# Performance work log

Measured on AMD Instinct MI355X. Metric: run time of the kernel, lower is better.

Reference implementation:

```python
import jax, jax.numpy as jnp
import numpy as np

DIM = 2048
N_HEADS = 32
N_KV_HEADS = 8
HEAD_DIM = 64
REPEATS = N_HEADS // N_KV_HEADS
SLIDING_WINDOW = 1024
EPS = 1e-6
B, T = 2, 2048


def _alibi_slopes(n):
    # n_heads=32 is a power of 2
    r = 2.0 ** (-8.0 / n)
    return jnp.asarray([r ** i for i in range(n)], dtype=jnp.float32)


def _rms_norm(x, w, eps):
    # RMSNorm over the last (flattened heads*head_dim) axis
    var = jnp.mean(x * x, axis=-1, keepdims=True)
    return x * jax.lax.rsqrt(var + eps) * w


def setup_inputs() -> dict:
    key = jax.random.key(0)
    ks = jax.random.split(key, 6)
    s = 0.02
    return {
        "x": jax.random.normal(ks[0], (B, T, DIM), jnp.float32),
        "wq": jax.random.normal(ks[1], (N_HEADS * HEAD_DIM, DIM), jnp.float32) * s,
        "wk": jax.random.normal(ks[2], (N_KV_HEADS * HEAD_DIM, DIM), jnp.float32) * s,
        "wv": jax.random.normal(ks[3], (N_KV_HEADS * HEAD_DIM, DIM), jnp.float32) * s,
        "wo": jax.random.normal(ks[4], (DIM, N_HEADS * HEAD_DIM), jnp.float32) * s,
        "q_norm_w": jnp.ones((N_HEADS * HEAD_DIM,), jnp.float32),
        "k_norm_w": jnp.ones((N_KV_HEADS * HEAD_DIM,), jnp.float32),
    }


def reference(x, wq, wk, wv, wo, q_norm_w, k_norm_w):
    bsz, seqlen, _ = x.shape
    xq = _rms_norm(x @ wq.T, q_norm_w, EPS)
    xk = _rms_norm(x @ wk.T, k_norm_w, EPS)
    xv = x @ wv.T
    xq = xq.reshape(bsz, seqlen, N_HEADS, HEAD_DIM).transpose(0, 2, 1, 3)  # b h t d
    xk = xk.reshape(bsz, seqlen, N_KV_HEADS, HEAD_DIM).transpose(0, 2, 1, 3)
    xv = xv.reshape(bsz, seqlen, N_KV_HEADS, HEAD_DIM).transpose(0, 2, 1, 3)
    # GQA: repeat_interleave kv heads
    xk = jnp.repeat(xk, REPEATS, axis=1)
    xv = jnp.repeat(xv, REPEATS, axis=1)

    pos = jnp.arange(seqlen)
    dist = pos[None, :] - pos[:, None]                     # [t,s] = s - t (<=0 on causal side)
    slopes = _alibi_slopes(N_HEADS)
    alibi = slopes[:, None, None] * dist.astype(jnp.float32)  # [h,t,s]
    allowed = (dist <= 0) & (dist >= -SLIDING_WINDOW)      # causal + sliding window
    bias = jnp.where(allowed[None], alibi, -jnp.inf)       # [h,t,s]

    scale = 1.0 / jnp.sqrt(jnp.asarray(HEAD_DIM, jnp.float32))
    scores = jnp.einsum("bhtd,bhsd->bhts", xq, xk) * scale + bias[None]
    attn = jax.nn.softmax(scores, axis=-1)
    out = jnp.einsum("bhts,bhsd->bhtd", attn, xv)          # [b,h,t,d]
    out = out.transpose(0, 2, 1, 3).reshape(bsz, seqlen, N_HEADS * HEAD_DIM)
    return out @ wo.T
```

## Files before the change

kernel.cpp:

```cpp
#include <hip/hip_runtime.h>


typedef _Float16 f16;
typedef __attribute__((ext_vector_type(8))) _Float16 f16x8;
typedef __attribute__((ext_vector_type(4))) _Float16 f16x4;
typedef __attribute__((ext_vector_type(4))) float f32x4;

#define T_ 2048
#define NH 32
#define NKV 8
#define HD 64
#define WINDOW 1024
#define EPS_ 1e-6f
#define LOG2E 1.44269504088896340736f
#define LDQKV 3072

__device__ inline void async16(void* lds, const void* g) {
  __builtin_amdgcn_global_load_lds(
      (const __attribute__((address_space(1))) unsigned int*)g,
      (__attribute__((address_space(3))) unsigned int*)lds, 16, 0, 0);
}

struct CvtArgs {
  const float* src[5];
  f16* dst[5];
  int n4[5];
};
__global__ __launch_bounds__(256) void cvt_multi(CvtArgs a) {
  const int seg = blockIdx.y;
  const float* in = a.src[seg];
  f16* out = a.dst[seg];
  const int n4 = a.n4[seg];
  for (int i = blockIdx.x * blockDim.x + threadIdx.x; i < n4;
       i += gridDim.x * blockDim.x) {
    float4 v = ((const float4*)in)[i];
    f16x4 o;
    o[0] = (f16)v.x; o[1] = (f16)v.y; o[2] = (f16)v.z; o[3] = (f16)v.w;
    ((f16x4*)out)[i] = o;
  }
}


#define DSRD(p, off) (*(const f16x8*)((p) + (off)))

#define LOADA(mh)                                                             \
  {                                                                           \
    _Pragma("unroll") for (int i = 0; i < 4; ++i) {                           \
      af[i][0] = DSRD(cA, bufo + abase + (mh) * 8192 + i * 2048 + xk0);       \
      af[i][1] = DSRD(cA, bufo + abase + (mh) * 8192 + i * 2048 + xk1);       \
    }                                                                         \
  }

#define LOADB(bfv, nh)                                                        \
  {                                                                           \
    _Pragma("unroll") for (int j = 0; j < 2; ++j) {                           \
      bfv[j][0] = DSRD(cB, bufo + bbase + (nh) * 4096 + j * 2048 + xk0);      \
      bfv[j][1] = DSRD(cB, bufo + bbase + (nh) * 4096 + j * 2048 + xk1);      \
    }                                                                         \
  }

#define FENCE_MFMA(mh, nh, bfv)                                               \
  {                                                                           \
    __builtin_amdgcn_s_barrier();                                             \
    asm volatile("s_waitcnt lgkmcnt(0)" ::: "memory");                        \
    __builtin_amdgcn_sched_barrier(0);                                        \
    __builtin_amdgcn_s_setprio(1);                                            \
    _Pragma("unroll") for (int i = 0; i < 4; ++i) {                           \
      _Pragma("unroll") for (int j = 0; j < 2; ++j) {                         \
        acc[(mh) * 4 + i][(nh) * 2 + j] =                                     \
            __builtin_amdgcn_mfma_f32_16x16x32_f16(                           \
                af[i][0], bfv[j][0], acc[(mh) * 4 + i][(nh) * 2 + j], 0, 0, 0); \
        acc[(mh) * 4 + i][(nh) * 2 + j] =                                     \
            __builtin_amdgcn_mfma_f32_16x16x32_f16(                           \
                af[i][1], bfv[j][1], acc[(mh) * 4 + i][(nh) * 2 + j], 0, 0, 0); \
      }                                                                       \
    }                                                                         \
    __builtin_amdgcn_s_setprio(0);                                            \
  }

__global__ __launch_bounds__(512, 2) void gemm_nt8(const f16* __restrict__ A,
                                                   const f16* __restrict__ B,
                                                   void* __restrict__ C,
                                                   int M, int N, int K, int ldc,
                                                   int out_f32) {
  extern __shared__ char smem[];
  f16* sA = (f16*)smem;
  f16* sB = (f16*)(smem + 65536);

  const int gx = gridDim.x;
  const int nwg = gx * gridDim.y;
  int bid = blockIdx.y * gx + blockIdx.x;
  if (!(nwg & 7)) bid = (bid & 7) * (nwg >> 3) + (bid >> 3);
  const int m0 = (bid / gx) * 256;
  const int n0 = (bid % gx) * 256;

  const int tid = threadIdx.x;
  const int lane = tid & 63;
  const int wave = tid >> 6;
  const int quad = lane >> 4, l16 = lane & 15;
  const int wm = wave >> 2, wn = wave & 3;

  const int srow = tid >> 3;
  const int sgr = (((tid & 7) ^ (srow & 7))) * 8;
  const f16* gA = A + (size_t)(m0 + srow) * K + sgr;
  const f16* gB = B + (size_t)(n0 + srow) * K + sgr;
  const size_t r64 = (size_t)64 * K;

  const char* cA = (const char*)sA;
  const char* cB = (const char*)sB;
  const int xm = (l16 & 7) << 4;
  const int xk0 = (quad * 16) ^ xm;
  const int xk1 = (64 + quad * 16) ^ xm;
  const int abase = (wm * 128 + l16) * 128;
  const int bbase = (wn * 64 + l16) * 128;

  f32x4 acc[8][4] = {};
  const int nt = K >> 6;

#pragma unroll
  for (int a = 0; a < 4; ++a) {
    async16(sA + a * 4096 + tid * 8, gA + (size_t)a * r64);
    async16(sB + a * 4096 + tid * 8, gB + (size_t)a * r64);
  }
  asm volatile("s_waitcnt vmcnt(0)" ::: "memory");
  __builtin_amdgcn_s_barrier();

  for (int t = 0; t < nt; ++t) {
    const int bufo = (t & 1) << 15;
    f16* sAn = sA + ((t & 1) ^ 1) * 16384;
    f16* sBn = sB + ((t & 1) ^ 1) * 16384;
    const bool st = (t + 1 < nt);
    const size_t gk = (size_t)(t + 1) * 64;

    f16x8 af[4][2], bf0[2][2], bf1[2][2];

    LOADA(0);
    LOADB(bf0, 0);
    if (st) {
      async16(sAn + 0 * 4096 + tid * 8, gA + 0 * r64 + gk);
      async16(sAn + 1 * 4096 + tid * 8, gA + 1 * r64 + gk);
      async16(sBn + 0 * 4096 + tid * 8, gB + 0 * r64 + gk);
      async16(sBn + 1 * 4096 + tid * 8, gB + 1 * r64 + gk);
    }
    FENCE_MFMA(0, 0, bf0);
    __builtin_amdgcn_s_barrier();

    LOADB(bf1, 1);
    if (st) {
      async16(sAn + 2 * 4096 + tid * 8, gA + 2 * r64 + gk);
      async16(sAn + 3 * 4096 + tid * 8, gA + 3 * r64 + gk);
      async16(sBn + 2 * 4096 + tid * 8, gB + 2 * r64 + gk);
      async16(sBn + 3 * 4096 + tid * 8, gB + 3 * r64 + gk);
    }
    FENCE_MFMA(0, 1, bf1);
    __builtin_amdgcn_s_barrier();

    LOADA(1);
    LOADB(bf0, 0);
    FENCE_MFMA(1, 0, bf0);
    __builtin_amdgcn_s_barrier();

    LOADB(bf1, 1);
    FENCE_MFMA(1, 1, bf1);
    if (st) asm volatile("s_waitcnt vmcnt(0)" ::: "memory");
    __builtin_amdgcn_s_barrier();
  }

#pragma unroll
  for (int im = 0; im < 8; ++im) {
    const int row0 = m0 + wm * 128 + im * 16 + quad * 4;
#pragma unroll
    for (int jn = 0; jn < 4; ++jn) {
      const int col = n0 + wn * 64 + jn * 16 + l16;
#pragma unroll
      for (int r = 0; r < 4; ++r) {
        const float v = acc[im][jn][r];
        if (out_f32) ((float*)C)[(size_t)(row0 + r) * ldc + col] = v;
        else         ((f16*)C)[(size_t)(row0 + r) * ldc + col] = (f16)v;
      }
    }
  }
}

__global__ __launch_bounds__(256) void rmsnorm2(f16* __restrict__ xqkv,
                                                const float* __restrict__ qw,
                                                const float* __restrict__ kw) {
  __shared__ float red[4];
  const int which = blockIdx.y;
  const int N = which ? 512 : 2048;
  const float* w = which ? kw : qw;
  f16* p = xqkv + (size_t)blockIdx.x * LDQKV + (which ? 2048 : 0);
  const int tid = threadIdx.x;
  const int per = N >> 8;
  float ss = 0.f;
#pragma unroll 4
  for (int i = 0; i < per; ++i) {
    const float v = (float)p[tid * per + i];
    ss += v * v;
  }
#pragma unroll
  for (int off = 32; off > 0; off >>= 1) ss += __shfl_down(ss, off);
  if ((tid & 63) == 0) red[tid >> 6] = ss;
  __syncthreads();
  const float scale = rsqrtf((red[0] + red[1] + red[2] + red[3]) / (float)N + EPS_);
#pragma unroll 4
  for (int i = 0; i < per; ++i) {
    const int c = tid * per + i;
    p[c] = (f16)((float)p[c] * scale * w[c]);
  }
}

__global__ __launch_bounds__(256) void vtrans(const f16* __restrict__ xqkv,
                                              f16* __restrict__ Vt) {
  __shared__ f16 L[64][72];
  const int t0 = blockIdx.x * 64;
  const int b = blockIdx.y >> 3, kh = blockIdx.y & 7;
  const int tid = threadIdx.x;
  const int r = tid >> 3, c = (tid & 7) * 8;
#pragma unroll
  for (int rp = 0; rp < 2; ++rp) {
    const int rr = r + rp * 32;
    *(f16x8*)(&L[rr][c]) =
        *(const f16x8*)(xqkv + (size_t)(b * T_ + t0 + rr) * LDQKV + 2560 + kh * 64 + c);
  }
  __syncthreads();
#pragma unroll
  for (int rp = 0; rp < 2; ++rp) {
    const int d = r + rp * 32;
    f16x8 o;
#pragma unroll
    for (int j = 0; j < 8; ++j) o[j] = L[c + j][d];
    *(f16x8*)(Vt + (size_t)((b * 8 + kh) * 64 + d) * T_ + t0 + c) = o;
  }
}

__global__ __launch_bounds__(256) void attn(const f16* __restrict__ Q,
                                            const f16* __restrict__ Kb,
                                            const f16* __restrict__ Vt_g,
                                            f16* __restrict__ O) {
  constexpr int LDW = 72;
  __shared__ f16 Qs[64 * LDW];
  __shared__ f16 Ks[64 * LDW];
  __shared__ f16 Vts[64 * LDW];
  __shared__ float Lx[4][16];

  const int qt = blockIdx.x, h = blockIdx.y, b = blockIdx.z;
  const int kh = h >> 2;
  const int q0 = qt * 64;
  const int tid = threadIdx.x;
  const int lane = tid & 63, wave = tid >> 6;
  const int quad = lane >> 4, l16 = lane & 15;
  const float scale2 = 0.125f * LOG2E;
  const float slope2 = exp2f(-0.25f * (float)h) * LOG2E;
  const float M2 = 10.0f;

  const int sr = tid >> 3, sc = (tid & 7) * 8;

#pragma unroll
  for (int rp = 0; rp < 2; ++rp) {
    const int rr = sr + rp * 32;
    *(f16x8*)(Qs + rr * LDW + sc) =
        *(const f16x8*)(Q + (size_t)(b * T_ + q0 + rr) * LDQKV + h * HD + sc);
  }
  __syncthreads();
  f16x8 qf[2];
#pragma unroll
  for (int kc = 0; kc < 2; ++kc)
    qf[kc] = *(const f16x8*)(Qs + (wave * 16 + l16) * LDW + kc * 32 + quad * 8);
  f16* Ps = Qs + wave * 16 * LDW;

  f32x4 o_acc[4] = {};
  float lsum = 0.f;

  const int kt_lo = (q0 >= WINDOW) ? ((q0 - WINDOW) >> 6) : 0;
  const int my_q = q0 + wave * 16 + l16;
  const size_t vbase = (size_t)((b * 8 + kh) * 64) * T_;

  float snbr[16];
#pragma unroll
  for (int nb = 0; nb < 4; ++nb)
#pragma unroll
    for (int r = 0; r < 4; ++r) snbr[nb * 4 + r] = slope2 * (float)(nb * 16 + r);
  float base = slope2 * (float)(kt_lo * 64 + quad * 4 - my_q) - M2;
  const float bstep = slope2 * 64.0f;

  f16x8 kreg[2], vreg[2];
  auto prefetch = [&](int k0) {
#pragma unroll
    for (int rp = 0; rp < 2; ++rp) {
      const int rr = sr + rp * 32;
      kreg[rp] = *(const f16x8*)(Kb + (size_t)(b * T_ + k0 + rr) * LDQKV + kh * HD + sc);
      vreg[rp] = *(const f16x8*)(Vt_g + vbase + (size_t)rr * T_ + k0 + sc);
    }
  };
  prefetch(kt_lo * 64);

  for (int kt = kt_lo; kt <= qt; ++kt) {
    const int k0 = kt * 64;
#pragma unroll
    for (int rp = 0; rp < 2; ++rp) {
      *(f16x8*)(Ks + (sr + rp * 32) * LDW + sc) = kreg[rp];
      *(f16x8*)(Vts + (sr + rp * 32) * LDW + sc) = vreg[rp];
    }
    __syncthreads();
    if (kt < qt) prefetch(k0 + 64);

    f32x4 s[4];
#pragma unroll
    for (int nb = 0; nb < 4; ++nb) {
      f32x4 a = {0.f, 0.f, 0.f, 0.f};
#pragma unroll
      for (int kc = 0; kc < 2; ++kc) {
        f16x8 kf = *(const f16x8*)(Ks + (nb * 16 + l16) * LDW + kc * 32 + quad * 8);
        a = __builtin_amdgcn_mfma_f32_16x16x32_f16(kf, qf[kc], a, 0, 0, 0);
      }
      s[nb] = a;
    }

    const bool maskt = (kt == qt) || (q0 + 63 - k0 > WINDOW);
#pragma unroll
    for (int nb = 0; nb < 4; ++nb) {
      f16x4 pk;
#pragma unroll
      for (int r = 0; r < 4; ++r) {
        float v = fmaf(s[nb][r], scale2, base + snbr[nb * 4 + r]);
        if (maskt) {
          const int dist = k0 + nb * 16 + quad * 4 + r - my_q;
          if (dist > 0 || dist < -WINDOW) v = -1e30f;
        }
        const float p = __builtin_amdgcn_exp2f(v);
        lsum += p;
        pk[r] = (f16)p;
      }
      *(f16x4*)(Ps + l16 * LDW + nb * 16 + quad * 4) = pk;
    }
    base += bstep;

#pragma unroll
    for (int nb = 0; nb < 4; ++nb) {
#pragma unroll
      for (int kc = 0; kc < 2; ++kc) {
        f16x8 pa = *(const f16x8*)(Ps + l16 * LDW + kc * 32 + quad * 8);
        f16x8 vb = *(const f16x8*)(Vts + (nb * 16 + l16) * LDW + kc * 32 + quad * 8);
        o_acc[nb] = __builtin_amdgcn_mfma_f32_16x16x32_f16(pa, vb, o_acc[nb], 0, 0, 0);
      }
    }
    __syncthreads();
  }

  lsum += __shfl_xor(lsum, 16);
  lsum += __shfl_xor(lsum, 32);
  if (quad == 0) Lx[wave][l16] = lsum;
  float rl[4];
#pragma unroll
  for (int r = 0; r < 4; ++r) rl[r] = 1.0f / Lx[wave][quad * 4 + r];

#pragma unroll
  for (int r = 0; r < 4; ++r) {
    const int q = q0 + wave * 16 + quad * 4 + r;
#pragma unroll
    for (int nb = 0; nb < 4; ++nb)
      O[(size_t)(b * T_ + q) * (NH * HD) + h * HD + nb * 16 + l16] =
          (f16)(o_acc[nb][r] * rl[r]);
  }
}

extern "C" void kernel_launch(void* const* d_in, const int* in_sizes, int n_in,
                              void* d_out, int out_size, void* d_ws, size_t ws_size,
                              hipStream_t stream) {
  const float* x  = (const float*)d_in[0];
  const float* wq = (const float*)d_in[1];
  const float* wk = (const float*)d_in[2];
  const float* wv = (const float*)d_in[3];
  const float* wo = (const float*)d_in[4];
  const float* qw = (const float*)d_in[5];
  const float* kw = (const float*)d_in[6];
  float* out = (float*)d_out;

  char* ws = (char*)d_ws;
  size_t off = 0;
  auto carve = [&](size_t bytes) -> char* {
    char* p = ws + off;
    off += (bytes + 255) & ~(size_t)255;
    return p;
  };
  f16* xh    = (f16*)carve((size_t)4096 * 2048 * 2);
  f16* wqkvh = (f16*)carve((size_t)3072 * 2048 * 2);
  f16* woh   = (f16*)carve((size_t)2048 * 2048 * 2);
  f16* xqkv  = (f16*)carve((size_t)4096 * 3072 * 2);
  f16* Vt = wqkvh + (size_t)2048 * 2048;
  f16* ao = xh;

  static bool attr_done = false;
  if (!attr_done) {
    (void)hipFuncSetAttribute((const void*)gemm_nt8,
                              hipFuncAttributeMaxDynamicSharedMemorySize,
                              131072);
    attr_done = true;
  }

  CvtArgs ca;
  ca.src[0] = x;  ca.dst[0] = xh;                            ca.n4[0] = (4096 * 2048) / 4;
  ca.src[1] = wq; ca.dst[1] = wqkvh;                         ca.n4[1] = (2048 * 2048) / 4;
  ca.src[2] = wk; ca.dst[2] = wqkvh + (size_t)2048 * 2048;   ca.n4[2] = (512 * 2048) / 4;
  ca.src[3] = wv; ca.dst[3] = wqkvh + (size_t)2560 * 2048;   ca.n4[3] = (512 * 2048) / 4;
  ca.src[4] = wo; ca.dst[4] = woh;                           ca.n4[4] = (2048 * 2048) / 4;
  cvt_multi<<<dim3(1024, 5), 256, 0, stream>>>(ca);

  gemm_nt8<<<dim3(12, 16), 512, 131072, stream>>>(xh, wqkvh, xqkv, 4096, 3072, 2048, LDQKV, 0);
  rmsnorm2<<<dim3(4096, 2), 256, 0, stream>>>(xqkv, qw, kw);
  vtrans<<<dim3(32, 16), 256, 0, stream>>>(xqkv, Vt);
  attn<<<dim3(32, 32, 2), 256, 0, stream>>>(xqkv, xqkv + 2048, Vt, ao);
  gemm_nt8<<<dim3(8, 16), 512, 131072, stream>>>(ao, woh, out, 4096, 2048, 2048, 2048, 1);
}
```

Baseline: 326.6 us.

## Pre-fragment K/V for attention, vectorize rmsnorm, and use 128-wide output GEMM tiles

A new kvfrag kernel writes K and V into MFMA-fragment order, so attention reads its operands straight from global memory with one 16-byte load per lane. This drops the shared-memory K/V staging and the per-tile __syncthreads. RMSNorm now uses vectorized f16x8/f16x2 loads with one element group per thread. The output projection GEMM is templated to BN=128, giving 256 workgroups instead of 128 to fill more CUs. Attention also gets a launch_bounds occupancy hint, at the cost of more global/L2 traffic per tile because K/V no longer go through LDS.

New measurement: 315.7 us. 1.03x faster.

```diff
diff --git a/kernel.cpp b/kernel.cpp
--- a/kernel.cpp
+++ b/kernel.cpp
@@ -4,6 +4,7 @@
 typedef _Float16 f16;
 typedef __attribute__((ext_vector_type(8))) _Float16 f16x8;
 typedef __attribute__((ext_vector_type(4))) _Float16 f16x4;
+typedef __attribute__((ext_vector_type(2))) _Float16 f16x2;
 typedef __attribute__((ext_vector_type(4))) float f32x4;
 
 #define T_ 2048
@@ -43,46 +44,16 @@
 
 #define DSRD(p, off) (*(const f16x8*)((p) + (off)))
 
-#define LOADA(mh)                                                             \
-  {                                                                           \
-    _Pragma("unroll") for (int i = 0; i < 4; ++i) {                           \
-      af[i][0] = DSRD(cA, bufo + abase + (mh) * 8192 + i * 2048 + xk0);       \
-      af[i][1] = DSRD(cA, bufo + abase + (mh) * 8192 + i * 2048 + xk1);       \
-    }                                                                         \
-  }
-
-#define LOADB(bfv, nh)                                                        \
-  {                                                                           \
-    _Pragma("unroll") for (int j = 0; j < 2; ++j) {                           \
-      bfv[j][0] = DSRD(cB, bufo + bbase + (nh) * 4096 + j * 2048 + xk0);      \
-      bfv[j][1] = DSRD(cB, bufo + bbase + (nh) * 4096 + j * 2048 + xk1);      \
-    }                                                                         \
-  }
-
-#define FENCE_MFMA(mh, nh, bfv)                                               \
-  {                                                                           \
-    __builtin_amdgcn_s_barrier();                                             \
-    asm volatile("s_waitcnt lgkmcnt(0)" ::: "memory");                        \
-    __builtin_amdgcn_sched_barrier(0);                                        \
-    __builtin_amdgcn_s_setprio(1);                                            \
-    _Pragma("unroll") for (int i = 0; i < 4; ++i) {                           \
-      _Pragma("unroll") for (int j = 0; j < 2; ++j) {                         \
-        acc[(mh) * 4 + i][(nh) * 2 + j] =                                     \
-            __builtin_amdgcn_mfma_f32_16x16x32_f16(                           \
-                af[i][0], bfv[j][0], acc[(mh) * 4 + i][(nh) * 2 + j], 0, 0, 0); \
-        acc[(mh) * 4 + i][(nh) * 2 + j] =                                     \
-            __builtin_amdgcn_mfma_f32_16x16x32_f16(                           \
-                af[i][1], bfv[j][1], acc[(mh) * 4 + i][(nh) * 2 + j], 0, 0, 0); \
-      }                                                                       \
-    }                                                                         \
-    __builtin_amdgcn_s_setprio(0);                                            \
-  }
-
+template <int BN>
 __global__ __launch_bounds__(512, 2) void gemm_nt8(const f16* __restrict__ A,
                                                    const f16* __restrict__ B,
                                                    void* __restrict__ C,
                                                    int M, int N, int K, int ldc,
                                                    int out_f32) {
+  constexpr int WN = BN / 4;
+  constexpr int JN = WN / 32;
+  constexpr int RB = BN / 64;
+  constexpr int BUFB = BN * 128;
   extern __shared__ char smem[];
   f16* sA = (f16*)smem;
   f16* sB = (f16*)(smem + 65536);
@@ -92,7 +63,7 @@
   int bid = blockIdx.y * gx + blockIdx.x;
   if (!(nwg & 7)) bid = (bid & 7) * (nwg >> 3) + (bid >> 3);
   const int m0 = (bid / gx) * 256;
-  const int n0 = (bid % gx) * 256;
+  const int n0 = (bid % gx) * BN;
 
   const int tid = threadIdx.x;
   const int lane = tid & 63;
@@ -112,56 +83,92 @@
   const int xk0 = (quad * 16) ^ xm;
   const int xk1 = (64 + quad * 16) ^ xm;
   const int abase = (wm * 128 + l16) * 128;
-  const int bbase = (wn * 64 + l16) * 128;
-
-  f32x4 acc[8][4] = {};
+  const int bbase = (wn * WN + l16) * 128;
+
+  f32x4 acc[8][2 * JN] = {};
   const int nt = K >> 6;
 
 #pragma unroll
-  for (int a = 0; a < 4; ++a) {
+  for (int a = 0; a < 4; ++a)
     async16(sA + a * 4096 + tid * 8, gA + (size_t)a * r64);
-    async16(sB + a * 4096 + tid * 8, gB + (size_t)a * r64);
-  }
+#pragma unroll
+  for (int rb = 0; rb < RB; ++rb)
+    async16(sB + rb * 4096 + tid * 8, gB + (size_t)rb * r64);
   asm volatile("s_waitcnt vmcnt(0)" ::: "memory");
   __builtin_amdgcn_s_barrier();
 
   for (int t = 0; t < nt; ++t) {
-    const int bufo = (t & 1) << 15;
-    f16* sAn = sA + ((t & 1) ^ 1) * 16384;
-    f16* sBn = sB + ((t & 1) ^ 1) * 16384;
+    const int bufoA = (t & 1) << 15;
+    const int bufoB = (t & 1) * BUFB;
+    f16* sAn = sA + (((t & 1) ^ 1) << 14);
+    f16* sBn = sB + ((t & 1) ^ 1) * (BUFB / 2);
     const bool st = (t + 1 < nt);
     const size_t gk = (size_t)(t + 1) * 64;
 
-    f16x8 af[4][2], bf0[2][2], bf1[2][2];
-
-    LOADA(0);
-    LOADB(bf0, 0);
+    f16x8 af[4][2], bf[JN][2];
+
+    auto ldA = [&](int mh) {
+#pragma unroll
+      for (int i = 0; i < 4; ++i) {
+        af[i][0] = DSRD(cA, bufoA + abase + mh * 8192 + i * 2048 + xk0);
+        af[i][1] = DSRD(cA, bufoA + abase + mh * 8192 + i * 2048 + xk1);
+      }
+    };
+    auto ldB = [&](int nh) {
+#pragma unroll
+      for (int j = 0; j < JN; ++j) {
+        bf[j][0] = DSRD(cB, bufoB + bbase + nh * (WN / 2) * 128 + j * 2048 + xk0);
+        bf[j][1] = DSRD(cB, bufoB + bbase + nh * (WN / 2) * 128 + j * 2048 + xk1);
+      }
+    };
+    auto mm = [&](int mh, int nh) {
+      __builtin_amdgcn_s_barrier();
+      asm volatile("s_waitcnt lgkmcnt(0)" ::: "memory");
+      __builtin_amdgcn_sched_barrier(0);
+      __builtin_amdgcn_s_setprio(1);
+#pragma unroll
+      for (int i = 0; i < 4; ++i) {
+#pragma unroll
+        for (int j = 0; j < JN; ++j) {
+          acc[mh * 4 + i][nh * JN + j] = __builtin_amdgcn_mfma_f32_16x16x32_f16(
+              af[i][0], bf[j][0], acc[mh * 4 + i][nh * JN + j], 0, 0, 0);
+          acc[mh * 4 + i][nh * JN + j] = __builtin_amdgcn_mfma_f32_16x16x32_f16(
+              af[i][1], bf[j][1], acc[mh * 4 + i][nh * JN + j], 0, 0, 0);
+        }
+      }
+      __builtin_amdgcn_s_setprio(0);
+    };
+
+    ldA(0); ldB(0);
     if (st) {
       async16(sAn + 0 * 4096 + tid * 8, gA + 0 * r64 + gk);
       async16(sAn + 1 * 4096 + tid * 8, gA + 1 * r64 + gk);
       async16(sBn + 0 * 4096 + tid * 8, gB + 0 * r64 + gk);
-      async16(sBn + 1 * 4096 + tid * 8, gB + 1 * r64 + gk);
+      if (RB == 4) async16(sBn + 1 * 4096 + tid * 8, gB + 1 * r64 + gk);
     }
-    FENCE_MFMA(0, 0, bf0);
+    mm(0, 0);
     __builtin_amdgcn_s_barrier();
 
-    LOADB(bf1, 1);
+    ldB(1);
     if (st) {
       async16(sAn + 2 * 4096 + tid * 8, gA + 2 * r64 + gk);
       async16(sAn + 3 * 4096 + tid * 8, gA + 3 * r64 + gk);
-      async16(sBn + 2 * 4096 + tid * 8, gB + 2 * r64 + gk);
-      async16(sBn + 3 * 4096 + tid * 8, gB + 3 * r64 + gk);
+      if (RB == 4) {
+        async16(sBn + 2 * 4096 + tid * 8, gB + 2 * r64 + gk);
+        async16(sBn + 3 * 4096 + tid * 8, gB + 3 * r64 + gk);
+      } else {
+        async16(sBn + 1 * 4096 + tid * 8, gB + 1 * r64 + gk);
+      }
     }
-    FENCE_MFMA(0, 1, bf1);
+    mm(0, 1);
     __builtin_amdgcn_s_barrier();
 
-    LOADA(1);
-    LOADB(bf0, 0);
-    FENCE_MFMA(1, 0, bf0);
+    ldA(1); ldB(0);
+    mm(1, 0);
     __builtin_amdgcn_s_barrier();
 
-    LOADB(bf1, 1);
-    FENCE_MFMA(1, 1, bf1);
+    ldB(1);
+    mm(1, 1);
     if (st) asm volatile("s_waitcnt vmcnt(0)" ::: "memory");
     __builtin_amdgcn_s_barrier();
   }
@@ -170,8 +177,8 @@
   for (int im = 0; im < 8; ++im) {
     const int row0 = m0 + wm * 128 + im * 16 + quad * 4;
 #pragma unroll
-    for (int jn = 0; jn < 4; ++jn) {
-      const int col = n0 + wn * 64 + jn * 16 + l16;
+    for (int jn = 0; jn < 2 * JN; ++jn) {
+      const int col = n0 + wn * WN + jn * 16 + l16;
 #pragma unroll
       for (int r = 0; r < 4; ++r) {
         const float v = acc[im][jn][r];
@@ -187,61 +194,83 @@
                                                 const float* __restrict__ kw) {
   __shared__ float red[4];
   const int which = blockIdx.y;
-  const int N = which ? 512 : 2048;
-  const float* w = which ? kw : qw;
-  f16* p = xqkv + (size_t)blockIdx.x * LDQKV + (which ? 2048 : 0);
   const int tid = threadIdx.x;
-  const int per = N >> 8;
-  float ss = 0.f;
-#pragma unroll 4
-  for (int i = 0; i < per; ++i) {
-    const float v = (float)p[tid * per + i];
-    ss += v * v;
-  }
-#pragma unroll
-  for (int off = 32; off > 0; off >>= 1) ss += __shfl_down(ss, off);
-  if ((tid & 63) == 0) red[tid >> 6] = ss;
-  __syncthreads();
-  const float scale = rsqrtf((red[0] + red[1] + red[2] + red[3]) / (float)N + EPS_);
-#pragma unroll 4
-  for (int i = 0; i < per; ++i) {
-    const int c = tid * per + i;
-    p[c] = (f16)((float)p[c] * scale * w[c]);
-  }
-}
-
-__global__ __launch_bounds__(256) void vtrans(const f16* __restrict__ xqkv,
-                                              f16* __restrict__ Vt) {
-  __shared__ f16 L[64][72];
-  const int t0 = blockIdx.x * 64;
+
+  auto block_sum = [&](float ss) -> float {
+#pragma unroll
+    for (int off = 32; off > 0; off >>= 1) ss += __shfl_down(ss, off);
+    if ((tid & 63) == 0) red[tid >> 6] = ss;
+    __syncthreads();
+    return red[0] + red[1] + red[2] + red[3];
+  };
+
+  if (which == 0) {
+    f16* p = xqkv + (size_t)blockIdx.x * LDQKV;
+    f16x8 v = ((const f16x8*)p)[tid];
+    float f[8];
+    float ss = 0.f;
+#pragma unroll
+    for (int j = 0; j < 8; ++j) { f[j] = (float)v[j]; ss += f[j] * f[j]; }
+    const float scale = rsqrtf(block_sum(ss) / 2048.0f + EPS_);
+    const float4 w0 = ((const float4*)qw)[tid * 2];
+    const float4 w1 = ((const float4*)qw)[tid * 2 + 1];
+    f16x8 o;
+    o[0] = (f16)(f[0] * scale * w0.x); o[1] = (f16)(f[1] * scale * w0.y);
+    o[2] = (f16)(f[2] * scale * w0.z); o[3] = (f16)(f[3] * scale * w0.w);
+    o[4] = (f16)(f[4] * scale * w1.x); o[5] = (f16)(f[5] * scale * w1.y);
+    o[6] = (f16)(f[6] * scale * w1.z); o[7] = (f16)(f[7] * scale * w1.w);
+    ((f16x8*)p)[tid] = o;
+  } else {
+    f16* p = xqkv + (size_t)blockIdx.x * LDQKV + 2048;
+    f16x2 v = ((const f16x2*)p)[tid];
+    const float f0 = (float)v[0], f1 = (float)v[1];
+    const float scale = rsqrtf(block_sum(f0 * f0 + f1 * f1) / 512.0f + EPS_);
+    const float2 w = ((const float2*)kw)[tid];
+    f16x2 o;
+    o[0] = (f16)(f0 * scale * w.x);
+    o[1] = (f16)(f1 * scale * w.y);
+    ((f16x2*)p)[tid] = o;
+  }
+}
+
+__global__ __launch_bounds__(256) void kvfrag(const f16* __restrict__ xqkv,
+                                              f16* __restrict__ Kf,
+                                              f16* __restrict__ Vf) {
+  __shared__ f16 Lk[64][72];
+  __shared__ f16 Lv[64][72];
+  const int kt = blockIdx.x;
   const int b = blockIdx.y >> 3, kh = blockIdx.y & 7;
+  const int t0 = kt * 64;
   const int tid = threadIdx.x;
   const int r = tid >> 3, c = (tid & 7) * 8;
 #pragma unroll
   for (int rp = 0; rp < 2; ++rp) {
     const int rr = r + rp * 32;
-    *(f16x8*)(&L[rr][c]) =
-        *(const f16x8*)(xqkv + (size_t)(b * T_ + t0 + rr) * LDQKV + 2560 + kh * 64 + c);
+    const f16* src = xqkv + (size_t)(b * T_ + t0 + rr) * LDQKV + kh * 64 + c;
+    *(f16x8*)(&Lk[rr][c]) = *(const f16x8*)(src + 2048);
+    *(f16x8*)(&Lv[rr][c]) = *(const f16x8*)(src + 2560);
   }
   __syncthreads();
-#pragma unroll
-  for (int rp = 0; rp < 2; ++rp) {
-    const int d = r + rp * 32;
+  const size_t obase = ((size_t)(b * 8 + kh) * 32 + kt) * 4096;
+#pragma unroll
+  for (int cc0 = 0; cc0 < 2; ++cc0) {
+    const int cc = tid + cc0 * 256;
+    const int nb = cc >> 7, kc = (cc >> 6) & 1, ln = cc & 63;
+    const int qd = ln >> 4, s16 = ln & 15;
+    *(f16x8*)(Kf + obase + cc * 8) = *(const f16x8*)(&Lk[nb * 16 + s16][kc * 32 + qd * 8]);
     f16x8 o;
 #pragma unroll
-    for (int j = 0; j < 8; ++j) o[j] = L[c + j][d];
-    *(f16x8*)(Vt + (size_t)((b * 8 + kh) * 64 + d) * T_ + t0 + c) = o;
-  }
-}
-
-__global__ __launch_bounds__(256) void attn(const f16* __restrict__ Q,
-                                            const f16* __restrict__ Kb,
-                                            const f16* __restrict__ Vt_g,
-                                            f16* __restrict__ O) {
+    for (int j = 0; j < 8; ++j) o[j] = Lv[kc * 32 + qd * 8 + j][nb * 16 + s16];
+    *(f16x8*)(Vf + obase + cc * 8) = o;
+  }
+}
+
+__global__ __launch_bounds__(256, 8) void attn(const f16* __restrict__ Q,
+                                               const f16* __restrict__ Kf,
+                                               const f16* __restrict__ Vf,
+                                               f16* __restrict__ O) {
   constexpr int LDW = 72;
   __shared__ f16 Qs[64 * LDW];
-  __shared__ f16 Ks[64 * LDW];
-  __shared__ f16 Vts[64 * LDW];
   __shared__ float Lx[4][16];
 
   const int qt = blockIdx.x, h = blockIdx.y, b = blockIdx.z;
@@ -274,56 +303,35 @@
 
   const int kt_lo = (q0 >= WINDOW) ? ((q0 - WINDOW) >> 6) : 0;
   const int my_q = q0 + wave * 16 + l16;
-  const size_t vbase = (size_t)((b * 8 + kh) * 64) * T_;
-
-  float snbr[16];
-#pragma unroll
-  for (int nb = 0; nb < 4; ++nb)
-#pragma unroll
-    for (int r = 0; r < 4; ++r) snbr[nb * 4 + r] = slope2 * (float)(nb * 16 + r);
+  const f16* kfb = Kf + (size_t)(b * 8 + kh) * 131072 + lane * 8;
+  const f16* vfb = Vf + (size_t)(b * 8 + kh) * 131072 + lane * 8;
+
+  float sr4[4];
+#pragma unroll
+  for (int r = 0; r < 4; ++r) sr4[r] = slope2 * (float)r;
   float base = slope2 * (float)(kt_lo * 64 + quad * 4 - my_q) - M2;
   const float bstep = slope2 * 64.0f;
-
-  f16x8 kreg[2], vreg[2];
-  auto prefetch = [&](int k0) {
-#pragma unroll
-    for (int rp = 0; rp < 2; ++rp) {
-      const int rr = sr + rp * 32;
-      kreg[rp] = *(const f16x8*)(Kb + (size_t)(b * T_ + k0 + rr) * LDQKV + kh * HD + sc);
-      vreg[rp] = *(const f16x8*)(Vt_g + vbase + (size_t)rr * T_ + k0 + sc);
-    }
-  };
-  prefetch(kt_lo * 64);
+  const float b16 = slope2 * 16.0f;
 
   for (int kt = kt_lo; kt <= qt; ++kt) {
     const int k0 = kt * 64;
-#pragma unroll
-    for (int rp = 0; rp < 2; ++rp) {
-      *(f16x8*)(Ks + (sr + rp * 32) * LDW + sc) = kreg[rp];
-      *(f16x8*)(Vts + (sr + rp * 32) * LDW + sc) = vreg[rp];
-    }
-    __syncthreads();
-    if (kt < qt) prefetch(k0 + 64);
-
-    f32x4 s[4];
+    const f16* kp = kfb + kt * 4096;
+    const f16* vp = vfb + kt * 4096;
+    const bool maskt = (kt == qt) || (q0 + 63 - k0 > WINDOW);
+
+    float bnb = base;
 #pragma unroll
     for (int nb = 0; nb < 4; ++nb) {
       f32x4 a = {0.f, 0.f, 0.f, 0.f};
 #pragma unroll
       for (int kc = 0; kc < 2; ++kc) {
-        f16x8 kf = *(const f16x8*)(Ks + (nb * 16 + l16) * LDW + kc * 32 + quad * 8);
-        a = __builtin_amdgcn_mfma_f32_16x16x32_f16(kf, qf[kc], a, 0, 0, 0);
-      }
-      s[nb] = a;
-    }
-
-    const bool maskt = (kt == qt) || (q0 + 63 - k0 > WINDOW);
-#pragma unroll
-    for (int nb = 0; nb < 4; ++nb) {
+        const f16x8 kfr = *(const f16x8*)(kp + (nb * 2 + kc) * 512);
+        a = __builtin_amdgcn_mfma_f32_16x16x32_f16(kfr, qf[kc], a, 0, 0, 0);
+      }
       f16x4 pk;
 #pragma unroll
       for (int r = 0; r < 4; ++r) {
-        float v = fmaf(s[nb][r], scale2, base + snbr[nb * 4 + r]);
+        float v = fmaf(a[r], scale2, bnb + sr4[r]);
         if (maskt) {
           const int dist = k0 + nb * 16 + quad * 4 + r - my_q;
           if (dist > 0 || dist < -WINDOW) v = -1e30f;
@@ -333,6 +341,7 @@
         pk[r] = (f16)p;
       }
       *(f16x4*)(Ps + l16 * LDW + nb * 16 + quad * 4) = pk;
+      bnb += b16;
     }
     base += bstep;
 
@@ -340,12 +349,11 @@
     for (int nb = 0; nb < 4; ++nb) {
 #pragma unroll
       for (int kc = 0; kc < 2; ++kc) {
-        f16x8 pa = *(const f16x8*)(Ps + l16 * LDW + kc * 32 + quad * 8);
-        f16x8 vb = *(const f16x8*)(Vts + (nb * 16 + l16) * LDW + kc * 32 + quad * 8);
+        const f16x8 pa = *(const f16x8*)(Ps + l16 * LDW + kc * 32 + quad * 8);
+        const f16x8 vb = *(const f16x8*)(vp + (nb * 2 + kc) * 512);
         o_acc[nb] = __builtin_amdgcn_mfma_f32_16x16x32_f16(pa, vb, o_acc[nb], 0, 0, 0);
       }
     }
-    __syncthreads();
   }
 
   lsum += __shfl_xor(lsum, 16);
@@ -388,14 +396,18 @@
   f16* wqkvh = (f16*)carve((size_t)3072 * 2048 * 2);
   f16* woh   = (f16*)carve((size_t)2048 * 2048 * 2);
   f16* xqkv  = (f16*)carve((size_t)4096 * 3072 * 2);
-  f16* Vt = wqkvh + (size_t)2048 * 2048;
+  f16* Kf = wqkvh;
+  f16* Vf = wqkvh + (size_t)16 * 131072;
   f16* ao = xh;
 
   static bool attr_done = false;
   if (!attr_done) {
-    (void)hipFuncSetAttribute((const void*)gemm_nt8,
+    (void)hipFuncSetAttribute((const void*)gemm_nt8<256>,
                               hipFuncAttributeMaxDynamicSharedMemorySize,
                               131072);
+    (void)hipFuncSetAttribute((const void*)gemm_nt8<128>,
+                              hipFuncAttributeMaxDynamicSharedMemorySize,
+                              98304);
     attr_done = true;
   }
 
@@ -407,9 +419,9 @@
   ca.src[4] = wo; ca.dst[4] = woh;                           ca.n4[4] = (2048 * 2048) / 4;
   cvt_multi<<<dim3(1024, 5), 256, 0, stream>>>(ca);
 
-  gemm_nt8<<<dim3(12, 16), 512, 131072, stream>>>(xh, wqkvh, xqkv, 4096, 3072, 2048, LDQKV, 0);
+  gemm_nt8<256><<<dim3(12, 16), 512, 131072, stream>>>(xh, wqkvh, xqkv, 4096, 3072, 2048, LDQKV, 0);
   rmsnorm2<<<dim3(4096, 2), 256, 0, stream>>>(xqkv, qw, kw);
-  vtrans<<<dim3(32, 16), 256, 0, stream>>>(xqkv, Vt);
-  attn<<<dim3(32, 32, 2), 256, 0, stream>>>(xqkv, xqkv + 2048, Vt, ao);
-  gemm_nt8<<<dim3(8, 16), 512, 131072, stream>>>(ao, woh, out, 4096, 2048, 2048, 2048, 1);
-}
+  kvfrag<<<dim3(32, 16), 256, 0, stream>>>(xqkv, Kf, Vf);
+  attn<<<dim3(32, 32, 2), 256, 0, stream>>>(xqkv, Kf, Vf, ao);
+  gemm_nt8<128><<<dim3(16, 16), 512, 98304, stream>>>(ao, woh, out, 4096, 2048, 2048, 2048, 1);
+}
```
